# Kernel tuning notes

Hardware: AMD Instinct MI355X
Metric: run time of the kernel (lower is better)

Reference implementation:

```python
import jax, jax.numpy as jnp
import numpy as np

CLP_K = 9
SCL_KS = (3, 4, 3)  # scl0_k, scl1_k, scl2_k from the source


def _ste(f, x):
    # straight-through estimator: forward f(x), identity gradient
    return x + jax.lax.stop_gradient(f(x) - x)


def floor_ste(x):
    return _ste(jnp.floor, x)


def round_ste(x):
    return _ste(jnp.round, x)


def conv_t(x, w, b):
    # torch F.conv_transpose2d with kernel 5, stride 2, padding 2, output_padding 1
    # expressed as an lhs-dilated conv; w is torch layout [in, out, kh, kw]
    k = w.shape[-1]
    wc = jnp.flip(w, axis=(-2, -1)).transpose(1, 0, 2, 3)  # -> [out, in, kh, kw]
    lo = k - 1 - 2           # k-1-padding = 2
    hi = k - 1 - 2 + 1       # + output_padding = 3
    y = jax.lax.conv_general_dilated(
        x, wc, window_strides=(1, 1), padding=[(lo, hi), (lo, hi)],
        lhs_dilation=(2, 2), dimension_numbers=('NCHW', 'OIHW', 'NCHW'))
    return y + b[None, :, None, None]


def split_deconv(x, w, b, split):
    # sum of `split` transposed convs with floor((round(W)+j)/split) quantized weights
    out = 0.0
    for j in range(split):
        wj = floor_ste((round_ste(w) + j) / split)
        bj = floor_ste((round_ste(b) + j) / split)
        out = out + conv_t(x, wj, bj)
    return out


def _g_s_forward(x, ws, bs, ms, relus, dv, Bits, split):
    # clp[i] = round((2^Bits - 1) / relus[i] * 2^(16+clp_k))
    clp = jnp.round((2.0 ** Bits - 1.0) / relus * 2.0 ** (16 + CLP_K))
    for i in range(3):
        x = split_deconv(x, ws[i], bs[i], split)
        x = x * ms[i][None, :, None, None]
        x = floor_ste((x + 2.0 ** (dv[i] - 1 - CLP_K)) / 2.0 ** (dv[i] - CLP_K))
        x = jnp.clip(x, 0.0, clp[i])
        sk = SCL_KS[i]
        scl = floor_ste((relus[i] + 2.0 ** (sk - 1)) / 2.0 ** sk)
        x = floor_ste((x * scl + 2.0 ** (15 + CLP_K - sk)) / 2.0 ** (16 + CLP_K - sk))
    x = split_deconv(x, ws[3], bs[3], split)
    x = x * ms[3][None, :, None, None]
    x = floor_ste((x + 2.0 ** (dv[3] - 9)) / 2.0 ** (dv[3] - 8))
    return x / 255.0


def setup_inputs() -> dict:
    key = jax.random.key(0)
    ks = jax.random.split(key, 16)
    N, M = 192, 320
    B, h, w = 1, 48, 48
    x = jax.random.randint(ks[0], (B, M, h, w), 0, 256).astype(jnp.float32)
    w1 = jax.random.normal(ks[1], (M, N, 5, 5), jnp.float32) * 20.0
    b1 = jax.random.normal(ks[2], (N,), jnp.float32) * 20.0
    w2 = jax.random.normal(ks[3], (N, N, 5, 5), jnp.float32) * 20.0
    b2 = jax.random.normal(ks[4], (N,), jnp.float32) * 20.0
    w3 = jax.random.normal(ks[5], (N, N, 5, 5), jnp.float32) * 20.0
    b3 = jax.random.normal(ks[6], (N,), jnp.float32) * 20.0
    w4 = jax.random.normal(ks[7], (N, 3, 5, 5), jnp.float32) * 20.0
    b4 = jax.random.normal(ks[8], (3,), jnp.float32) * 20.0
    muls0 = jax.random.randint(ks[9], (N,), 1, 1000).astype(jnp.float32)
    muls1 = jax.random.randint(ks[10], (N,), 1, 1000).astype(jnp.float32)
    muls2 = jax.random.randint(ks[11], (N,), 1, 1000).astype(jnp.float32)
    muls3 = jax.random.randint(ks[12], (3,), 1, 1000).astype(jnp.float32)
    relus = jnp.array([40000.0, 36000.0, 30000.0], jnp.float32)
    muls_dvds = jnp.array([24, 24, 24, 24], jnp.int32)
    return {"x": x, "w1": w1, "b1": b1, "w2": w2, "b2": b2, "w3": w3,
            "b3": b3, "w4": w4, "b4": b4, "muls0": muls0, "muls1": muls1,
            "muls2": muls2, "muls3": muls3, "relus": relus,
            "muls_dvds": muls_dvds, "Bits": 8, "split": 4}


def reference(x, w1, b1, w2, b2, w3, b3, w4, b4,
              muls0, muls1, muls2, muls3, relus, muls_dvds, Bits, split):
    dv = muls_dvds.astype(jnp.float32)
    ws = (w1, w2, w3, w4)
    bs = (b1, b2, b3, b4)
    ms = (muls0, muls1, muls2, muls3)
    return _g_s_forward(x, ws, bs, ms, relus, dv, int(Bits), int(split))
```

## Files before the change

kernel.cpp:

```cpp
#include <hip/hip_runtime.h>
#include <cmath>


typedef int int4v  __attribute__((ext_vector_type(4)));
typedef int int16v __attribute__((ext_vector_type(16)));

#define GLOBAL_AS __attribute__((address_space(1)))
#define LDS_AS    __attribute__((address_space(3)))

__device__ __forceinline__ void dma16(const signed char* g, signed char* l) {
    __builtin_amdgcn_global_load_lds((const GLOBAL_AS int*)g, (LDS_AS int*)l,
                                     16, 0, 0);
}

__device__ __forceinline__ void tap_to_k(int t, int& ky, int& kx) {
    if (t < 9)       { int dy = t/3,  dx = t%3;                   ky = 4-2*dy; kx = 4-2*dx; }
    else if (t < 15) { int u = t-9;   int dy = u/2, dx = 1+(u&1);  ky = 4-2*dy; kx = 5-2*dx; }
    else if (t < 21) { int u = t-15;  int dy = 1+u/3, dx = u%3;    ky = 5-2*dy; kx = 4-2*dx; }
    else             { int u = t-21;  int dy = 1+u/2, dx = 1+(u&1); ky = 5-2*dy; kx = 5-2*dx; }
}

__global__ __launch_bounds__(256)
void prep_all(const float* __restrict__ x, signed char* __restrict__ xh,
              const float* __restrict__ w1, const float* __restrict__ w2,
              const float* __restrict__ w3, const float* __restrict__ w4,
              signed char* __restrict__ p1, signed char* __restrict__ p2,
              signed char* __restrict__ p3, signed char* __restrict__ p4,
              int* __restrict__ t1, int* __restrict__ t2,
              int* __restrict__ t3, int* __restrict__ t4) {
    __shared__ __align__(16) signed char smem[26112];
    const int bid = blockIdx.x;
    const int tid = threadIdx.x;

    if (bid < 180) {
        float (*t)[65] = (float(*)[65])smem;
        const int C = 320, HW = 48 * 48;
        const int p0 = (bid % 36) * 64;
        const int c0 = (bid / 36) * 64;
        const int pL = tid & 63;
        const int r0 = tid >> 6;
        #pragma unroll
        for (int k = 0; k < 16; ++k) {
            int ciL = r0 * 16 + k;
            t[ciL][pL] = x[(size_t)(c0 + ciL) * HW + p0 + pL];
        }
        __syncthreads();
        #pragma unroll
        for (int k = 0; k < 16; ++k) {
            int pL2 = r0 * 16 + k;
            xh[(size_t)(p0 + pL2) * C + c0 + pL] = (signed char)((int)t[pL][pL2] - 128);
        }
    } else if (bid < 312) {
        int u = bid - 180;
        int layer, s;
        if (u < 60)      { layer = 0; s = u; }
        else if (u < 96) { layer = 1; s = u - 60; }
        else             { layer = 2; s = u - 96; }
        const float* w = (layer == 0) ? w1 : (layer == 1) ? w2 : w3;
        signed char* out = (layer == 0) ? p1 : (layer == 1) ? p2 : p3;
        int* ts = (layer == 0) ? t1 : (layer == 1) ? t2 : t3;
        const int Cout = 192;
        const int qs = s / 6, nb = s % 6;

        signed char* ls = smem;
        int (*lsum)[32] = (int(*)[32])(smem + 25600);
        if (tid < 128) ((int*)lsum)[tid] = 0;
        __syncthreads();

        #pragma unroll
        for (int k = 0; k < 4; ++k) {
            const int pidx = tid + k * 256;
            const int cil = pidx >> 5;
            const int colp = pidx & 31;
            const int ci = qs * 32 + cil;
            const int cop = nb * 32 + colp;
            const float* wr = w + (size_t)(ci * Cout + cop) * 25;
            const int halfp = cil >> 4, j = cil & 15;
            const int base = (halfp * 32 + colp) * 16 + j;
            int psum[4] = {0, 0, 0, 0};
            #pragma unroll
            for (int tt = 0; tt < 25; ++tt) {
                int ky, kx; tap_to_k(tt, ky, kx);
                float v = rintf(wr[ky * 5 + kx]);
                v = fminf(fmaxf(v, -128.0f), 127.0f);
                int iv = (int)v;
                ls[tt * 1024 + base] = (signed char)iv;
                psum[((ky & 1) << 1) | (kx & 1)] += iv;
            }
            #pragma unroll
            for (int p = 0; p < 4; ++p) atomicAdd(&lsum[p][colp], psum[p]);
        }
        __syncthreads();

        signed char* dst = out + (size_t)s * 25600;
        for (int i = tid; i < 1600; i += 256)
            *(int4v*)&dst[i * 16] = *(const int4v*)&ls[i * 16];
        if (tid < 128) {
            const int p = tid >> 5, colp = tid & 31;
            atomicAdd(&ts[p * Cout + nb * 32 + colp], lsum[p][colp]);
        }
    } else if (bid < 366) {
        const int bx = bid - 312;
        #pragma unroll
        for (int k = 0; k < 4; ++k) {
            int idx = bx * 1024 + k * 256 + tid;
            int j    = idx & 15;
            int lane = (idx >> 4) & 63;
            int rem  = idx >> 10;
            int s9   = rem % 9;
            int qs   = rem / 9;
            int colp = lane & 31;
            int cop  = colp & 7;
            int p    = colp >> 3;
            int py = p >> 1, px = p & 1;
            int dy = s9 / 3, dx = s9 % 3;
            int ci = qs * 32 + ((lane >> 5) << 4) + j;
            bool part = (py == 0 || dy >= 1) && (px == 0 || dx >= 1);
            float v = 0.0f;
            if (cop < 3 && part) {
                int ky = py ? 5 - 2 * dy : 4 - 2 * dy;
                int kx = px ? 5 - 2 * dx : 4 - 2 * dx;
                v = rintf(w4[(size_t)(ci * 3 + cop) * 25 + ky * 5 + kx]);
                v = fminf(fmaxf(v, -128.0f), 127.0f);
            }
            p4[idx] = (signed char)(int)v;
        }
    } else if (tid < 128) {
        const int Cin = 192, Cout = 3;
        const int u = (bid - 366) * 2 + (tid >> 6);
        const int lane = tid & 63;
        const int cop = u % Cout, p = u / Cout;
        const int py = p >> 1, px = p & 1;
        const int nky = (5 - py + 1) >> 1;
        const int nkx = (5 - px + 1) >> 1;
        const int ntap = nky * nkx;
        int sacc = 0;
        for (int idx = lane; idx < Cin * ntap; idx += 64) {
            const int ci = idx / ntap;
            const int uu = idx - ci * ntap;
            const int ky = py + 2 * (uu / nkx);
            const int kx = px + 2 * (uu % nkx);
            float v = rintf(w4[(size_t)(ci * Cout + cop) * 25 + ky * 5 + kx]);
            v = fminf(fmaxf(v, -128.0f), 127.0f);
            sacc += (int)v;
        }
        #pragma unroll
        for (int off = 32; off > 0; off >>= 1)
            sacc += __shfl_down(sacc, off, 64);
        if (lane == 0) t4[u] = sacc;
    }
}

__device__ __forceinline__ constexpr int role_nt(int role, int s9) {
    constexpr int NT0[9] = {1,1,1,1,2,2,1,2,2};
    constexpr int NT1[9] = {0,1,1,1,2,2,1,2,2};
    return role == 0 ? NT0[s9] : NT1[s9];
}
__device__ __forceinline__ constexpr int role_tap(int role, int s9, int u) {
    constexpr int T0[9][2] = {{0,0},{1,0},{2,0},{3,0},{4,21},{5,22},{6,0},{7,23},{8,24}};
    constexpr int T1[9][2] = {{0,0},{9,0},{10,0},{15,0},{11,16},{12,17},{18,0},{13,19},{14,20}};
    return role == 0 ? T0[s9][u] : T1[s9][u];
}
__device__ __forceinline__ constexpr int role_acc(int role, int s9, int u) {
    constexpr int A0[9][2] = {{0,0},{0,0},{0,0},{0,0},{0,1},{0,1},{0,0},{0,1},{0,1}};
    constexpr int A1[9][2] = {{0,0},{0,0},{0,0},{1,0},{0,1},{0,1},{1,0},{0,1},{0,1}};
    return role == 0 ? A0[s9][u] : A1[s9][u];
}

template<int ROLE, int R>
__device__ __forceinline__ void compute_role(const signed char* xsb, const signed char* bsb,
                                             int16v (&acc)[R][2], const int (&p0)[R],
                                             int half, int lane) {
    #pragma unroll
    for (int s9 = 0; s9 < 9; ++s9) {
        if (role_nt(ROLE, s9) == 0) continue;
        const int dy = s9 / 3, dx = s9 % 3;
        int4v a[R];
        #pragma unroll
        for (int r = 0; r < R; ++r)
            a[r] = *(const int4v*)&xsb[(p0[r] + dy * 18 + dx) * 32 + half * 16];
        #pragma unroll
        for (int u = 0; u < 2; ++u) {
            if (u < role_nt(ROLE, s9)) {
                int4v b = *(const int4v*)&bsb[role_tap(ROLE, s9, u) * 1024 + lane * 16];
                const int ai = role_acc(ROLE, s9, u);
                #pragma unroll
                for (int r = 0; r < R; ++r)
                    acc[r][ai] = __builtin_amdgcn_mfma_i32_32x32x32_i8(a[r], b, acc[r][ai], 0, 0, 0);
            }
        }
    }
}

template<int MW, int R, bool BDBUF, int TAG>
__global__ __launch_bounds__(MW * 64, 4)
void deconv_v16(const signed char* __restrict__ xin, const signed char* __restrict__ wpk,
                const float* __restrict__ bias, const float* __restrict__ muls,
                const int* __restrict__ tsum,
                const float* __restrict__ relus, const int* __restrict__ dvds,
                const int* __restrict__ bitsp, const signed char* __restrict__ xpad,
                int layer, int Cin, int Cout, int NT, int Hq, int Wq,
                int NB, int NQX, int T8,
                signed char* __restrict__ outp) {
    constexpr int PAIRS = MW / 2;
    constexpr int QROWS = PAIRS * R * 2;
    constexpr int NROW = QROWS + 2;
    constexpr int NPIX = NROW * 18;
    constexpr int THREADS = MW * 64;
    constexpr int XC = NPIX * 2;
    constexpr int XI = (XC + THREADS - 1) / THREADS;
    constexpr int BC = 1600;
    constexpr int BI = (BC + THREADS - 1) / THREADS;
    constexpr int NBS = BDBUF ? 2 : 1;

    __shared__ __align__(16) signed char xs[2][NPIX * 32];
    __shared__ __align__(16) signed char bs[NBS][25600];

    const int tid  = threadIdx.x;
    const int lane = tid & 63;
    const int wid  = tid >> 6;
    const int pairId = wid >> 1;
    const int role   = wid & 1;

    int nb, qx, qy;
    {
        const int bi = blockIdx.x;
        if (T8 > 0) {
            const int xcd = bi & 7, j = bi >> 3;
            const int tl = j / NB, n = j - tl * NB;
            const int tile = xcd * T8 + tl;
            nb = n; qx = tile % NQX; qy = tile / NQX;
        } else {
            nb = bi % NB;
            const int s = bi / NB;
            qx = s % NQX; qy = s / NQX;
        }
    }
    const int qx0 = qx * 16;
    const int qy0 = qy * QROWS;
    const int n0  = nb * 32;

    int16v acc[R][2];
    #pragma unroll
    for (int r = 0; r < R; ++r)
        #pragma unroll
        for (int p = 0; p < 2; ++p)
            #pragma unroll
            for (int e = 0; e < 16; ++e) acc[r][p][e] = 0;

    const int half   = lane >> 5;
    const int rowbit = (lane >> 4) & 1;
    const int col    = lane & 15;
    int p0[R];
    #pragma unroll
    for (int r = 0; r < R; ++r)
        p0[r] = ((pairId * R + r) * 2 + rowbit) * 18 + col;

    const signed char* xsrc[XI];
    #pragma unroll
    for (int t = 0; t < XI; ++t) {
        int i = tid + t * THREADS;
        xsrc[t] = xpad;
        if (i < XC) {
            int pix = i >> 1, g = i & 1;
            int rr = pix / 18, cc = pix - rr * 18;
            int y = qy0 - 1 + rr, xx = qx0 - 1 + cc;
            bool ok = (unsigned)y < (unsigned)Hq && (unsigned)xx < (unsigned)Wq;
            xsrc[t] = ok ? (xin + ((size_t)y * Wq + xx) * Cin + g * 16)
                         : (xpad + g * 16);
        }
    }

    auto dma_x = [&](int ck, int b) {
        #pragma unroll
        for (int t = 0; t < XI; ++t) {
            int i = tid + t * THREADS;
            if (i < XC) dma16(xsrc[t] + ck, &xs[b][i * 16]);
        }
    };
    auto dma_b = [&](int cs, int b) {
        const signed char* ws = wpk + (size_t)(cs * NT + nb) * 25600;
        #pragma unroll
        for (int t = 0; t < BI; ++t) {
            int i = tid + t * THREADS;
            if (i < BC) dma16(ws + (size_t)i * 16, &bs[b][i * 16]);
        }
    };

    dma_x(0, 0);
    if (BDBUF) dma_b(0, 0);
    for (int ck = 0, s = 0; ck < Cin; ck += 32, ++s) {
        const int cb = s & 1;
        if (BDBUF) {
            __syncthreads();
            if (ck + 32 < Cin) {
                dma_x((s + 1) * 32, cb ^ 1);
                dma_b(s + 1, cb ^ 1);
            }
            if (role == 0) compute_role<0, R>(xs[cb], bs[cb], acc, p0, half, lane);
            else           compute_role<1, R>(xs[cb], bs[cb], acc, p0, half, lane);
        } else {
            __syncthreads();
            dma_b(s, 0);
            if (ck + 32 < Cin) dma_x((s + 1) * 32, cb ^ 1);
            __syncthreads();
            if (role == 0) compute_role<0, R>(xs[cb], bs[0], acc, p0, half, lane);
            else           compute_role<1, R>(xs[cb], bs[0], acc, p0, half, lane);
        }
    }

    const int dv = dvds[layer];
    float add1 = ldexpf(1.0f, dv - 10);
    float inv1 = ldexpf(1.0f, -(dv - 9));
    const float relu = relus[layer];
    const int sk = (layer == 1) ? 4 : 3;
    const float bitsv = ldexpf(1.0f, bitsp[0]) - 1.0f;
    float clp, scl;
    {
        #pragma clang fp contract(off)
        clp = rintf(bitsv / relu * 33554432.0f);
        scl = floorf((relu + ldexpf(1.0f, sk - 1)) * ldexpf(1.0f, -sk));
    }
    float add2 = ldexpf(1.0f, 24 - sk);
    float inv2 = ldexpf(1.0f, -(25 - sk));

    const int co = n0 + (lane & 31);
    float bq = rintf(bias[co]);
    float mm = muls[co];
    int pmap[2];
    pmap[0] = role == 0 ? 0 : 1;
    pmap[1] = role == 0 ? 3 : 2;
    int fullp[2];
    #pragma unroll
    for (int a = 0; a < 2; ++a) fullp[a] = tsum[pmap[a] * Cout + co];

    const int Wout = Wq * 2;

    #pragma unroll
    for (int r = 0; r < R; ++r) {
        #pragma unroll
        for (int a = 0; a < 2; ++a) {
            const int p = pmap[a];
            const int py = p >> 1, px = p & 1;
            #pragma unroll
            for (int reg = 0; reg < 16; ++reg) {
                const int mrow = (reg & 3) + 8 * (reg >> 2) + 4 * (lane >> 5);
                const int qy2 = qy0 + (pairId * R + r) * 2 + (mrow >> 4);
                const int qx2 = qx0 + (mrow & 15);
                float v = (float)(acc[r][a][reg] + 128 * fullp[a]);
                {
                    #pragma clang fp contract(off)
                    v = (v + bq) * mm;
                    v = floorf((v + add1) * inv1);
                    v = fminf(fmaxf(v, 0.0f), clp);
                    v = floorf((v * scl + add2) * inv2);
                }
                const int oy = 2 * qy2 + py, ox = 2 * qx2 + px;
                outp[((size_t)oy * Wout + ox) * Cout + co] = (signed char)((int)v - 128);
            }
        }
    }
}

__global__ __launch_bounds__(256, 4)
void deconv_final_v16(const signed char* __restrict__ xin, const signed char* __restrict__ wpk,
                      const float* __restrict__ bias, const float* __restrict__ muls,
                      const int* __restrict__ tsum, const int* __restrict__ dvds,
                      const signed char* __restrict__ xpad,
                      int Cin, int Hq, int Wq, float* __restrict__ outp) {
    constexpr int R = 2, MW = 4;
    constexpr int QROWS = MW * R * 2;
    constexpr int NROW = QROWS + 2;
    constexpr int NPIX = NROW * 18;
    constexpr int THREADS = 256;
    constexpr int XC = NPIX * 2;
    constexpr int XI = (XC + THREADS - 1) / THREADS;
    constexpr int BC = 576;
    constexpr int BI = (BC + THREADS - 1) / THREADS;

    __shared__ __align__(16) signed char xs[2][NPIX * 32];
    __shared__ __align__(16) signed char bs[2][9216];

    const int tid  = threadIdx.x;
    const int lane = tid & 63;
    const int wid  = tid >> 6;
    const int qx0  = blockIdx.y * 16;
    const int qy0  = blockIdx.z * QROWS;

    int16v acc[R];
    #pragma unroll
    for (int r = 0; r < R; ++r)
        #pragma unroll
        for (int e = 0; e < 16; ++e) acc[r][e] = 0;

    const int half   = lane >> 5;
    const int rowbit = (lane >> 4) & 1;
    const int col    = lane & 15;
    int p0[R];
    #pragma unroll
    for (int r = 0; r < R; ++r)
        p0[r] = ((wid * R + r) * 2 + rowbit) * 18 + col;

    const signed char* xsrc[XI];
    #pragma unroll
    for (int t = 0; t < XI; ++t) {
        int i = tid + t * THREADS;
        xsrc[t] = xpad;
        if (i < XC) {
            int pix = i >> 1, g = i & 1;
            int rr = pix / 18, cc = pix - rr * 18;
            int y = qy0 - 1 + rr, xx = qx0 - 1 + cc;
            bool ok = (unsigned)y < (unsigned)Hq && (unsigned)xx < (unsigned)Wq;
            xsrc[t] = ok ? (xin + ((size_t)y * Wq + xx) * Cin + g * 16)
                         : (xpad + g * 16);
        }
    }

    auto dma_x = [&](int ck, int b) {
        #pragma unroll
        for (int t = 0; t < XI; ++t) {
            int i = tid + t * THREADS;
            if (i < XC) dma16(xsrc[t] + ck, &xs[b][i * 16]);
        }
    };
    auto dma_b = [&](int cs, int b) {
        const signed char* ws = wpk + (size_t)cs * 9216;
        #pragma unroll
        for (int t = 0; t < BI; ++t) {
            int i = tid + t * THREADS;
            if (i < BC) dma16(ws + (size_t)i * 16, &bs[b][i * 16]);
        }
    };

    dma_x(0, 0);
    dma_b(0, 0);
    for (int ck = 0; ck < Cin; ck += 32) {
        const int cb = (ck >> 5) & 1;
        __syncthreads();
        if (ck + 32 < Cin) {
            dma_x(ck + 32, cb ^ 1);
            dma_b((ck >> 5) + 1, cb ^ 1);
        }
        #pragma unroll
        for (int s9 = 0; s9 < 9; ++s9) {
            const int dy = s9 / 3, dx = s9 % 3;
            int4v b = *(const int4v*)&bs[cb][s9 * 1024 + lane * 16];
            #pragma unroll
            for (int r = 0; r < R; ++r) {
                int4v a = *(const int4v*)&xs[cb][(p0[r] + dy * 18 + dx) * 32 + half * 16];
                acc[r] = __builtin_amdgcn_mfma_i32_32x32x32_i8(a, b, acc[r], 0, 0, 0);
            }
        }
    }

    const int dv = dvds[3];
    const float add1 = ldexpf(1.0f, dv - 9);
    const float inv1 = ldexpf(1.0f, -(dv - 8));

    const int coln = lane & 31;
    const int co = coln & 7;
    const int p  = coln >> 3;
    const int py = p >> 1, px = p & 1;
    const bool valid = (co < 3);
    float bq = 0.f, mm = 0.f;
    int fp = 0;
    if (valid) { bq = rintf(bias[co]); mm = muls[co]; fp = tsum[p * 3 + co]; }

    const int Wout = Wq * 2, Hout = Hq * 2;
    #pragma unroll
    for (int r = 0; r < R; ++r) {
        #pragma unroll
        for (int reg = 0; reg < 16; ++reg) {
            const int mrow = (reg & 3) + 8 * (reg >> 2) + 4 * (lane >> 5);
            const int qy = qy0 + (wid * R + r) * 2 + (mrow >> 4);
            const int qx = qx0 + (mrow & 15);
            float v = (float)(acc[r][reg] + 128 * fp);
            {
                #pragma clang fp contract(off)
                v = (v + bq) * mm;
                v = floorf((v + add1) * inv1);
                v = v / 255.0f;
            }
            if (valid) {
                const int oy = 2 * qy + py, ox = 2 * qx + px;
                outp[((size_t)co * Hout + oy) * Wout + ox] = v;
            }
        }
    }
}

extern "C" void kernel_launch(void* const* d_in, const int* in_sizes, int n_in,
                              void* d_out, int out_size, void* d_ws, size_t ws_size,
                              hipStream_t stream) {
    const float* x  = (const float*)d_in[0];
    const float* w1 = (const float*)d_in[1];
    const float* b1 = (const float*)d_in[2];
    const float* w2 = (const float*)d_in[3];
    const float* b2 = (const float*)d_in[4];
    const float* w3 = (const float*)d_in[5];
    const float* b3 = (const float*)d_in[6];
    const float* w4 = (const float*)d_in[7];
    const float* b4 = (const float*)d_in[8];
    const float* m0 = (const float*)d_in[9];
    const float* m1 = (const float*)d_in[10];
    const float* m2 = (const float*)d_in[11];
    const float* m3 = (const float*)d_in[12];
    const float* relus = (const float*)d_in[13];
    const int* dvds = (const int*)d_in[14];
    const int* bitsp = (const int*)d_in[15];

    signed char* wsb = (signed char*)d_ws;
    size_t o = 0;
    signed char* wpk1 = wsb + o; o += (size_t)10 * 6 * 25600;
    signed char* wpk2 = wsb + o; o += (size_t)6 * 6 * 25600;
    signed char* wpk3 = wsb + o; o += (size_t)6 * 6 * 25600;
    signed char* wpk4 = wsb + o; o += (size_t)6 * 9216;
    int* ts1 = (int*)(wsb + o); o += 4 * 192 * 4;
    int* ts2 = (int*)(wsb + o); o += 4 * 192 * 4;
    int* ts3 = (int*)(wsb + o); o += 4 * 192 * 4;
    int* ts4 = (int*)(wsb + o); o += 4 * 4 * 4;
    const size_t zbytes = 3 * (4 * 192 * 4) + 4 * 4 * 4;
    o = (o + 15) & ~(size_t)15;
    signed char* xpad = wsb + o; o += 512;
    signed char* xh = wsb + o; o += (size_t)48 * 48 * 320;
    signed char* a1 = wsb + o; o += (size_t)96 * 96 * 192;
    signed char* a2 = wsb + o; o += (size_t)192 * 192 * 192;
    signed char* a3 = wsb + o; o += (size_t)384 * 384 * 192;

    hipMemsetAsync(ts1, 0, zbytes, stream);
    hipMemsetAsync(xpad, 0x80, 512, stream);

    prep_all<<<372, 256, 0, stream>>>(x, xh, w1, w2, w3, w4,
                                      wpk1, wpk2, wpk3, wpk4,
                                      ts1, ts2, ts3, ts4);

    deconv_v16<4, 1, true, 0><<<216, 256, 0, stream>>>(
        xh, wpk1, b1, m0, ts1, relus, dvds, bitsp, xpad, 0, 320, 192, 6, 48, 48,
        6, 3, 0, a1);
    deconv_v16<4, 2, false, 1><<<432, 256, 0, stream>>>(
        a1, wpk2, b2, m1, ts2, relus, dvds, bitsp, xpad, 1, 192, 192, 6, 96, 96,
        6, 6, 0, a2);
    deconv_v16<4, 2, false, 2><<<1728, 256, 0, stream>>>(
        a2, wpk3, b3, m2, ts3, relus, dvds, bitsp, xpad, 2, 192, 192, 6, 192, 192,
        6, 12, 36, a3);
    deconv_final_v16<<<dim3(1, 24, 24), 256, 0, stream>>>(
        a3, wpk4, b4, m3, ts4, dvds, xpad, 192, 384, 384, (float*)d_out);
}
```

Measured before the change: 196.9 us.

## Drop memsets via per-slice partial sums and stage final output through LDS

Weight-sum partials are now written per input-channel slice instead of atomically accumulated, so the zeroing memset is removed and consumers sum the slices. The xpad fill is moved into prep_all, removing the second memset. The final deconv stages its strided float outputs in LDS and writes them back as coalesced rows. This trades two memset launches and scattered stores for a few extra loads per block and an extra LDS round trip.

```diff
diff --git a/kernel.cpp b/kernel.cpp
--- a/kernel.cpp
+++ b/kernel.cpp
@@ -26,8 +26,9 @@
               const float* __restrict__ w3, const float* __restrict__ w4,
               signed char* __restrict__ p1, signed char* __restrict__ p2,
               signed char* __restrict__ p3, signed char* __restrict__ p4,
-              int* __restrict__ t1, int* __restrict__ t2,
-              int* __restrict__ t3, int* __restrict__ t4) {
+              int* __restrict__ tsp1, int* __restrict__ tsp2,
+              int* __restrict__ tsp3, int* __restrict__ t4,
+              int* __restrict__ xpadw) {
     __shared__ __align__(16) signed char smem[26112];
     const int bid = blockIdx.x;
     const int tid = threadIdx.x;
@@ -58,7 +59,7 @@
         else             { layer = 2; s = u - 96; }
         const float* w = (layer == 0) ? w1 : (layer == 1) ? w2 : w3;
         signed char* out = (layer == 0) ? p1 : (layer == 1) ? p2 : p3;
-        int* ts = (layer == 0) ? t1 : (layer == 1) ? t2 : t3;
+        int* tsp = (layer == 0) ? tsp1 : (layer == 1) ? tsp2 : tsp3;
         const int Cout = 192;
         const int qs = s / 6, nb = s % 6;
 
@@ -97,7 +98,7 @@
             *(int4v*)&dst[i * 16] = *(const int4v*)&ls[i * 16];
         if (tid < 128) {
             const int p = tid >> 5, colp = tid & 31;
-            atomicAdd(&ts[p * Cout + nb * 32 + colp], lsum[p][colp]);
+            tsp[(qs * 4 + p) * Cout + nb * 32 + colp] = lsum[p][colp];
         }
     } else if (bid < 366) {
         const int bx = bid - 312;
@@ -125,29 +126,33 @@
             }
             p4[idx] = (signed char)(int)v;
         }
-    } else if (tid < 128) {
-        const int Cin = 192, Cout = 3;
-        const int u = (bid - 366) * 2 + (tid >> 6);
-        const int lane = tid & 63;
-        const int cop = u % Cout, p = u / Cout;
-        const int py = p >> 1, px = p & 1;
-        const int nky = (5 - py + 1) >> 1;
-        const int nkx = (5 - px + 1) >> 1;
-        const int ntap = nky * nkx;
-        int sacc = 0;
-        for (int idx = lane; idx < Cin * ntap; idx += 64) {
-            const int ci = idx / ntap;
-            const int uu = idx - ci * ntap;
-            const int ky = py + 2 * (uu / nkx);
-            const int kx = px + 2 * (uu % nkx);
-            float v = rintf(w4[(size_t)(ci * Cout + cop) * 25 + ky * 5 + kx]);
-            v = fminf(fmaxf(v, -128.0f), 127.0f);
-            sacc += (int)v;
-        }
-        #pragma unroll
-        for (int off = 32; off > 0; off >>= 1)
-            sacc += __shfl_down(sacc, off, 64);
-        if (lane == 0) t4[u] = sacc;
+    } else {
+        if (tid < 128) {
+            const int Cin = 192, Cout = 3;
+            const int u = (bid - 366) * 2 + (tid >> 6);
+            const int lane = tid & 63;
+            const int cop = u % Cout, p = u / Cout;
+            const int py = p >> 1, px = p & 1;
+            const int nky = (5 - py + 1) >> 1;
+            const int nkx = (5 - px + 1) >> 1;
+            const int ntap = nky * nkx;
+            int sacc = 0;
+            for (int idx = lane; idx < Cin * ntap; idx += 64) {
+                const int ci = idx / ntap;
+                const int uu = idx - ci * ntap;
+                const int ky = py + 2 * (uu / nkx);
+                const int kx = px + 2 * (uu % nkx);
+                float v = rintf(w4[(size_t)(ci * Cout + cop) * 25 + ky * 5 + kx]);
+                v = fminf(fmaxf(v, -128.0f), 127.0f);
+                sacc += (int)v;
+            }
+            #pragma unroll
+            for (int off = 32; off > 0; off >>= 1)
+                sacc += __shfl_down(sacc, off, 64);
+            if (lane == 0) t4[u] = sacc;
+        } else if (bid == 366) {
+            xpadw[tid - 128] = (int)0x80808080;
+        }
     }
 }
 
@@ -194,9 +199,9 @@
 
 template<int MW, int R, bool BDBUF, int TAG>
 __global__ __launch_bounds__(MW * 64, 4)
-void deconv_v16(const signed char* __restrict__ xin, const signed char* __restrict__ wpk,
+void deconv_v17(const signed char* __restrict__ xin, const signed char* __restrict__ wpk,
                 const float* __restrict__ bias, const float* __restrict__ muls,
-                const int* __restrict__ tsum,
+                const int* __restrict__ tsp, int QS,
                 const float* __restrict__ relus, const int* __restrict__ dvds,
                 const int* __restrict__ bitsp, const signed char* __restrict__ xpad,
                 int layer, int Cin, int Cout, int NT, int Hq, int Wq,
@@ -330,9 +335,11 @@
     int pmap[2];
     pmap[0] = role == 0 ? 0 : 1;
     pmap[1] = role == 0 ? 3 : 2;
-    int fullp[2];
-    #pragma unroll
-    for (int a = 0; a < 2; ++a) fullp[a] = tsum[pmap[a] * Cout + co];
+    int fullp[2] = {0, 0};
+    for (int q = 0; q < QS; ++q) {
+        fullp[0] += tsp[(q * 4 + pmap[0]) * Cout + co];
+        fullp[1] += tsp[(q * 4 + pmap[1]) * Cout + co];
+    }
 
     const int Wout = Wq * 2;
 
@@ -363,7 +370,7 @@
 }
 
 __global__ __launch_bounds__(256, 4)
-void deconv_final_v16(const signed char* __restrict__ xin, const signed char* __restrict__ wpk,
+void deconv_final_v17(const signed char* __restrict__ xin, const signed char* __restrict__ wpk,
                       const float* __restrict__ bias, const float* __restrict__ muls,
                       const int* __restrict__ tsum, const int* __restrict__ dvds,
                       const signed char* __restrict__ xpad,
@@ -377,9 +384,12 @@
     constexpr int XI = (XC + THREADS - 1) / THREADS;
     constexpr int BC = 576;
     constexpr int BI = (BC + THREADS - 1) / THREADS;
-
-    __shared__ __align__(16) signed char xs[2][NPIX * 32];
-    __shared__ __align__(16) signed char bs[2][9216];
+    constexpr int XBUF = NPIX * 32;
+
+    __shared__ __align__(16) signed char smem[2 * XBUF + 2 * 9216];
+    signed char (*xs)[XBUF] = (signed char(*)[XBUF])smem;
+    signed char (*bs)[9216] = (signed char(*)[9216])(smem + 2 * XBUF);
+    float* obuf = (float*)smem;
 
     const int tid  = threadIdx.x;
     const int lane = tid & 63;
@@ -466,14 +476,15 @@
     int fp = 0;
     if (valid) { bq = rintf(bias[co]); mm = muls[co]; fp = tsum[p * 3 + co]; }
 
-    const int Wout = Wq * 2, Hout = Hq * 2;
+    __syncthreads();
+
     #pragma unroll
     for (int r = 0; r < R; ++r) {
         #pragma unroll
         for (int reg = 0; reg < 16; ++reg) {
             const int mrow = (reg & 3) + 8 * (reg >> 2) + 4 * (lane >> 5);
-            const int qy = qy0 + (wid * R + r) * 2 + (mrow >> 4);
-            const int qx = qx0 + (mrow & 15);
+            const int lq_y = (wid * R + r) * 2 + (mrow >> 4);
+            const int lq_x = mrow & 15;
             float v = (float)(acc[r][reg] + 128 * fp);
             {
                 #pragma clang fp contract(off)
@@ -482,10 +493,22 @@
                 v = v / 255.0f;
             }
             if (valid) {
-                const int oy = 2 * qy + py, ox = 2 * qx + px;
-                outp[((size_t)co * Hout + oy) * Wout + ox] = v;
-            }
-        }
+                const int ly = 2 * lq_y + py, lx = 2 * lq_x + px;
+                obuf[co * 1024 + ly * 32 + lx] = v;
+            }
+        }
+    }
+    __syncthreads();
+
+    const int Wout = Wq * 2, Hout = Hq * 2;
+    const int oyb = qy0 * 2, oxb = qx0 * 2;
+    #pragma unroll
+    for (int k = 0; k < 12; ++k) {
+        const int idx = tid + k * 256;
+        const int c  = idx >> 10;
+        const int rem = idx & 1023;
+        const int ly = rem >> 5, lx = rem & 31;
+        outp[((size_t)c * Hout + oyb + ly) * Wout + oxb + lx] = obuf[idx];
     }
 }
 
@@ -515,11 +538,10 @@
     signed char* wpk2 = wsb + o; o += (size_t)6 * 6 * 25600;
     signed char* wpk3 = wsb + o; o += (size_t)6 * 6 * 25600;
     signed char* wpk4 = wsb + o; o += (size_t)6 * 9216;
-    int* ts1 = (int*)(wsb + o); o += 4 * 192 * 4;
-    int* ts2 = (int*)(wsb + o); o += 4 * 192 * 4;
-    int* ts3 = (int*)(wsb + o); o += 4 * 192 * 4;
-    int* ts4 = (int*)(wsb + o); o += 4 * 4 * 4;
-    const size_t zbytes = 3 * (4 * 192 * 4) + 4 * 4 * 4;
+    int* tsp1 = (int*)(wsb + o); o += 10 * 4 * 192 * 4;
+    int* tsp2 = (int*)(wsb + o); o += 6 * 4 * 192 * 4;
+    int* tsp3 = (int*)(wsb + o); o += 6 * 4 * 192 * 4;
+    int* ts4  = (int*)(wsb + o); o += 4 * 4 * 4;
     o = (o + 15) & ~(size_t)15;
     signed char* xpad = wsb + o; o += 512;
     signed char* xh = wsb + o; o += (size_t)48 * 48 * 320;
@@ -527,22 +549,19 @@
     signed char* a2 = wsb + o; o += (size_t)192 * 192 * 192;
     signed char* a3 = wsb + o; o += (size_t)384 * 384 * 192;
 
-    hipMemsetAsync(ts1, 0, zbytes, stream);
-    hipMemsetAsync(xpad, 0x80, 512, stream);
-
     prep_all<<<372, 256, 0, stream>>>(x, xh, w1, w2, w3, w4,
                                       wpk1, wpk2, wpk3, wpk4,
-                                      ts1, ts2, ts3, ts4);
-
-    deconv_v16<4, 1, true, 0><<<216, 256, 0, stream>>>(
-        xh, wpk1, b1, m0, ts1, relus, dvds, bitsp, xpad, 0, 320, 192, 6, 48, 48,
+                                      tsp1, tsp2, tsp3, ts4, (int*)xpad);
+
+    deconv_v17<4, 1, true, 0><<<216, 256, 0, stream>>>(
+        xh, wpk1, b1, m0, tsp1, 10, relus, dvds, bitsp, xpad, 0, 320, 192, 6, 48, 48,
         6, 3, 0, a1);
-    deconv_v16<4, 2, false, 1><<<432, 256, 0, stream>>>(
-        a1, wpk2, b2, m1, ts2, relus, dvds, bitsp, xpad, 1, 192, 192, 6, 96, 96,
+    deconv_v17<4, 2, false, 1><<<432, 256, 0, stream>>>(
+        a1, wpk2, b2, m1, tsp2, 6, relus, dvds, bitsp, xpad, 1, 192, 192, 6, 96, 96,
         6, 6, 0, a2);
-    deconv_v16<4, 2, false, 2><<<1728, 256, 0, stream>>>(
-        a2, wpk3, b3, m2, ts3, relus, dvds, bitsp, xpad, 2, 192, 192, 6, 192, 192,
+    deconv_v17<4, 2, false, 2><<<1728, 256, 0, stream>>>(
+        a2, wpk3, b3, m2, tsp3, 6, relus, dvds, bitsp, xpad, 2, 192, 192, 6, 192, 192,
         6, 12, 36, a3);
-    deconv_final_v16<<<dim3(1, 24, 24), 256, 0, stream>>>(
+    deconv_final_v17<<<dim3(1, 24, 24), 256, 0, stream>>>(
         a3, wpk4, b4, m3, ts4, dvds, xpad, 192, 384, 384, (float*)d_out);
 }
```

After: 193.9 us. No clear change (-1.5%).
